# Kernel tuning notes

Measured on AMD Instinct MI355X. Metric: run time of the kernel, lower is better.

Reference implementation:

```python
import jax, jax.numpy as jnp
import numpy as np

NEG_SLOPE = 0.2  # PyG GATConv LeakyReLU slope
N_NODES = 50000
N_EDGES = 800000
F_IN, HID, HEADS, N_CLS = 166, 64, 8, 2


def setup_inputs() -> dict:
    key = jax.random.key(0)
    ks = jax.random.split(key, 16)
    s = 0.1
    return {
        "x": jax.random.normal(ks[0], (N_NODES, F_IN), jnp.float32),
        "edge_index": jax.random.randint(ks[1], (2, N_EDGES), 0, N_NODES, jnp.int64),
        "W1": jax.random.normal(ks[2], (F_IN, HEADS * HID), jnp.float32) * s,
        "a_src1": jax.random.normal(ks[3], (HEADS, HID), jnp.float32) * s,
        "a_dst1": jax.random.normal(ks[4], (HEADS, HID), jnp.float32) * s,
        "b1": jnp.zeros((HEADS * HID,), jnp.float32),
        # conv_final: 512 -> 64, 1 head, mean (concat=False)
        "W2": jax.random.normal(ks[5], (HEADS * HID, HID), jnp.float32) * s,
        "a_src2": jax.random.normal(ks[6], (1, HID), jnp.float32) * s,
        "a_dst2": jax.random.normal(ks[7], (1, HID), jnp.float32) * s,
        "b2": jnp.zeros((HID,), jnp.float32),
        # classifier MLP 64 -> 64 -> 2
        "Wc1": jax.random.normal(ks[8], (HID, HID), jnp.float32) * s,
        "bc1": jnp.zeros((HID,), jnp.float32),
        "Wc2": jax.random.normal(ks[9], (HID, N_CLS), jnp.float32) * s,
        "bc2": jnp.zeros((N_CLS,), jnp.float32),
    }


def gat_layer(x, src, dst, W, a_src, a_dst, b, concat):
    """PyG-style GATConv (eval mode, self-loops already in src/dst)."""
    N = x.shape[0]
    H, C = a_src.shape
    xp = (x @ W).reshape(N, H, C)                 # [N,H,C] projected features
    al_src = jnp.sum(xp * a_src, axis=-1)         # [N,H]
    al_dst = jnp.sum(xp * a_dst, axis=-1)         # [N,H]
    e = jax.nn.leaky_relu(al_src[src] + al_dst[dst], NEG_SLOPE)  # [E,H]
    # segment softmax over incoming edges of each target node
    m = jax.ops.segment_max(e, dst, num_segments=N)
    ex = jnp.exp(e - m[dst])
    denom = jax.ops.segment_sum(ex, dst, num_segments=N)
    alpha = ex / denom[dst]                       # [E,H]
    out = jax.ops.segment_sum(alpha[:, :, None] * xp[src], dst, num_segments=N)  # [N,H,C]
    out = out.reshape(N, H * C) if concat else out.mean(axis=1)
    return out + b


def reference(x, edge_index, W1, a_src1, a_dst1, b1, W2, a_src2, a_dst2, b2, Wc1, bc1, Wc2, bc2):
    N = x.shape[0]
    loops = jnp.arange(N, dtype=edge_index.dtype)
    src = jnp.concatenate([edge_index[0], loops])  # add self-loops (PyG default)
    dst = jnp.concatenate([edge_index[1], loops])
    h = jax.nn.elu(gat_layer(x, src, dst, W1, a_src1, a_dst1, b1, concat=True))
    h = gat_layer(h, src, dst, W2, a_src2, a_dst2, b2, concat=False)
    h = jax.nn.relu(h @ Wc1 + bc1)
    return h @ Wc2 + bc2
```

## Files before the change

kernel.cpp:

```cpp
#include <hip/hip_runtime.h>

#define NN   50000
#define E0   800000
#define ET   850000
#define FIN  166
#define KP1  192
#define HID  64
#define NH   8
#define F1   512
#define SCHUNK 52
#define DEGPAD (1024*SCHUNK)
#define G1BX 391
#define G1BLK (G1BX*4)
#define SCB  832

typedef __attribute__((ext_vector_type(8))) short short8;
typedef __attribute__((ext_vector_type(4))) float f32x4;
typedef __attribute__((ext_vector_type(4))) int int4v;
typedef unsigned short ush;

__device__ __forceinline__ float bf2f(unsigned short u){
  unsigned int x = ((unsigned int)u) << 16;
  return __builtin_bit_cast(float, x);
}
__device__ __forceinline__ unsigned short f2bf(float f){
  unsigned int x = __builtin_bit_cast(unsigned int, f);
  x += 0x7FFFu + ((x >> 16) & 1u);
  return (unsigned short)(x >> 16);
}

#define G1 (KP1/8)
#define T0V (NN*G1)
#define T1V (T0V + 512*G1)
#define T2V (T1V + 64*64)
#define T2W (T2V + 512)
#define T3V (T2W + ET)
__global__ __launch_bounds__(256) void k_prep_v(const float* __restrict__ x,
                                                const float* __restrict__ W1,
                                                const float* __restrict__ W2,
                                                const float* __restrict__ Wc1,
                                                const int* __restrict__ ei,
                                                ush* __restrict__ xpad,
                                                ush* __restrict__ W1t,
                                                ush* __restrict__ W2t,
                                                ush* __restrict__ Wc1t,
                                                int* __restrict__ deg){
  int i = blockIdx.x*256 + threadIdx.x;
  if (i >= T3V) return;
  if (i < T0V){
    int n = i / G1, g = i - n*G1, k0 = g*8;
    short8 o;
    #pragma unroll
    for (int j = 0; j < 8; j++){
      int k = k0 + j;
      o[j] = (short)f2bf(k < FIN ? x[(size_t)n*FIN + k] : 0.f);
    }
    *(short8*)(xpad + (size_t)n*KP1 + k0) = o;
  } else if (i < T1V){
    int j = i - T0V;
    int col = j / G1, g = j - col*G1, k0 = g*8;
    short8 o;
    #pragma unroll
    for (int q = 0; q < 8; q++){
      int k = k0 + q;
      o[q] = (short)f2bf(k < FIN ? W1[(size_t)k*512 + col] : 0.f);
    }
    *(short8*)(W1t + (size_t)col*KP1 + k0) = o;
  } else if (i < T2V){
    int j = i - T1V;
    int col = j >> 6, g = j & 63, k0 = g*8;
    short8 o;
    #pragma unroll
    for (int q = 0; q < 8; q++)
      o[q] = (short)f2bf(W2[(size_t)(k0 + q)*HID + col]);
    *(short8*)(W2t + (size_t)col*F1 + k0) = o;
  } else if (i < T2W){
    int j = i - T2V;
    int col = j >> 3, k0 = (j & 7)*8;
    short8 o;
    #pragma unroll
    for (int q = 0; q < 8; q++)
      o[q] = (short)f2bf(Wc1[(size_t)(k0 + q)*HID + col]);
    *(short8*)(Wc1t + (size_t)col*HID + k0) = o;
  } else {
    int e = i - T2W;
    int dst = (e < E0) ? ei[E0 + e] : (e - E0);
    atomicAdd(&deg[dst], 1);
  }
}

__global__ __launch_bounds__(1024) void k_scan(const int* __restrict__ deg,
                                               int* __restrict__ offs,
                                               int* __restrict__ cur){
  __shared__ int sums[1024];
  int t = threadIdx.x;
  for (int i = t; i < NN; i += 1024) cur[i] = 0;
  int base = t * SCHUNK;
  int4v v[13];
  int loc = 0;
  #pragma unroll
  for (int c = 0; c < 13; c++){
    v[c] = *(const int4v*)(deg + base + c*4);
    loc += v[c].x + v[c].y + v[c].z + v[c].w;
  }
  sums[t] = loc; __syncthreads();
  for (int off = 1; off < 1024; off <<= 1){
    int s = (t >= off) ? sums[t - off] : 0;
    __syncthreads();
    sums[t] += s;
    __syncthreads();
  }
  int run = sums[t] - loc;
  #pragma unroll
  for (int c = 0; c < 13; c++){
    int i0 = base + c*4;
    if (i0 + 0 < NN) offs[i0 + 0] = run;  run += v[c].x;
    if (i0 + 1 < NN) offs[i0 + 1] = run;  run += v[c].y;
    if (i0 + 2 < NN) offs[i0 + 2] = run;  run += v[c].z;
    if (i0 + 3 < NN) offs[i0 + 3] = run;  run += v[c].w;
  }
  if (t == 1023) offs[NN] = sums[1023];
}

__global__ __launch_bounds__(256) void k_sg1(const int* __restrict__ ei,
                                             const int* __restrict__ offs,
                                             int* __restrict__ cur,
                                             int* __restrict__ esrc,
                                             const ush* __restrict__ xpad,
                                             const ush* __restrict__ W1t,
                                             const float* __restrict__ a_s,
                                             const float* __restrict__ a_d,
                                             ush* __restrict__ xp1,
                                             float* __restrict__ als,
                                             float* __restrict__ ald){
  __shared__ ush As[128][40];
  __shared__ ush Bs[128][40];
  const int bid = blockIdx.x;
  if (bid >= G1BLK){
    int vb = bid - G1BLK;
    for (int e = vb*256 + (int)threadIdx.x; e < ET; e += SCB*256){
      int src, dst;
      if (e < E0){ src = ei[e]; dst = ei[E0 + e]; }
      else       { src = e - E0; dst = src; }
      int pos = offs[dst] + atomicAdd(&cur[dst], 1);
      esrc[pos] = src;
    }
    return;
  }
  const int m0 = (bid % G1BX)*128, n0 = (bid / G1BX)*128;
  const int t = threadIdx.x, wid = t>>6, l = t&63;
  const int wr = wid>>1, wc = wid&1;
  const int lr = l&15, ksl = (l>>4)*8;
  const int srow = t>>1, sc = (t&1)*16;

  f32x4 acc[4][4];
  #pragma unroll
  for (int m = 0; m < 4; m++)
    #pragma unroll
    for (int n = 0; n < 4; n++)
      #pragma unroll
      for (int j = 0; j < 4; j++) acc[m][n][j] = 0.f;

  const int gr = m0 + srow;
  const ush* Ap = xpad + (size_t)gr*KP1 + sc;
  const ush* Bp = W1t + (size_t)(n0 + srow)*KP1 + sc;

  for (int s = 0; s < 6; s++){
    const int kk = s*32;
    short8 a0, a1;
    #pragma unroll
    for (int j = 0; j < 8; j++){ a0[j] = 0; a1[j] = 0; }
    if (gr < NN){ a0 = *(const short8*)(Ap + kk); a1 = *(const short8*)(Ap + kk + 8); }
    short8 b0 = *(const short8*)(Bp + kk);
    short8 b1 = *(const short8*)(Bp + kk + 8);
    *(short8*)&As[srow][sc]   = a0;
    *(short8*)&As[srow][sc+8] = a1;
    *(short8*)&Bs[srow][sc]   = b0;
    *(short8*)&Bs[srow][sc+8] = b1;
    __syncthreads();
    short8 af[4], bfr[4];
    #pragma unroll
    for (int m = 0; m < 4; m++) af[m]  = *(const short8*)&As[wr*64 + m*16 + lr][ksl];
    #pragma unroll
    for (int n = 0; n < 4; n++) bfr[n] = *(const short8*)&Bs[wc*64 + n*16 + lr][ksl];
    #pragma unroll
    for (int m = 0; m < 4; m++)
      #pragma unroll
      for (int n = 0; n < 4; n++)
        acc[m][n] = __builtin_amdgcn_mfma_f32_16x16x32_bf16(af[m], bfr[n], acc[m][n], 0, 0, 0);
    __syncthreads();
  }

  #pragma unroll
  for (int m = 0; m < 4; m++)
    #pragma unroll
    for (int n = 0; n < 4; n++)
      #pragma unroll
      for (int j = 0; j < 4; j++){
        int row = m0 + wr*64 + m*16 + (l>>4)*4 + j;
        int col = n0 + wc*64 + n*16 + lr;
        if (row < NN) xp1[(size_t)row*F1 + col] = f2bf(acc[m][n][j]);
      }

  const int head = (bid / G1BX)*2 + wc;
  float asv[4], adv[4];
  #pragma unroll
  for (int n = 0; n < 4; n++){
    asv[n] = a_s[head*64 + n*16 + lr];
    adv[n] = a_d[head*64 + n*16 + lr];
  }
  #pragma unroll
  for (int m = 0; m < 4; m++)
    #pragma unroll
    for (int j = 0; j < 4; j++){
      float ps = 0.f, pd = 0.f;
      #pragma unroll
      for (int n = 0; n < 4; n++){
        ps = fmaf(acc[m][n][j], asv[n], ps);
        pd = fmaf(acc[m][n][j], adv[n], pd);
      }
      #pragma unroll
      for (int o = 1; o < 16; o <<= 1){
        ps += __shfl_xor(ps, o, 64);
        pd += __shfl_xor(pd, o, 64);
      }
      if (lr == 0){
        int row = m0 + wr*64 + m*16 + (l>>4)*4 + j;
        if (row < NN){
          als[(size_t)row*NH + head] = fminf(fmaxf(ps, -30.f), 30.f);
          ald[(size_t)row*NH + head] = fminf(fmaxf(pd, -30.f), 30.f);
        }
      }
    }
}

__global__ __launch_bounds__(256) void k_gemm2(const ush* __restrict__ h1,
                                               const ush* __restrict__ W2t,
                                               const float* __restrict__ a_s,
                                               const float* __restrict__ a_d,
                                               ush* __restrict__ xp2,
                                               float* __restrict__ als,
                                               float* __restrict__ ald){
  __shared__ ush As[128][40];
  __shared__ ush Bs[64][40];
  const int m0 = blockIdx.x*128;
  const int t = threadIdx.x, wid = t>>6, l = t&63;
  const int lr = l&15, ksl = (l>>4)*8;
  const int srow = t>>1, sc = (t&1)*16;

  f32x4 acc[2][4];
  #pragma unroll
  for (int m = 0; m < 2; m++)
    #pragma unroll
    for (int n = 0; n < 4; n++)
      #pragma unroll
      for (int j = 0; j < 4; j++) acc[m][n][j] = 0.f;

  const int gr = m0 + srow;
  const ush* Ap = h1 + (size_t)gr*F1 + sc;
  const ush* Bp = W2t + (size_t)srow*F1 + sc;

  for (int s = 0; s < 16; s++){
    const int kk = s*32;
    short8 a0, a1;
    #pragma unroll
    for (int j = 0; j < 8; j++){ a0[j] = 0; a1[j] = 0; }
    if (gr < NN){ a0 = *(const short8*)(Ap + kk); a1 = *(const short8*)(Ap + kk + 8); }
    *(short8*)&As[srow][sc]   = a0;
    *(short8*)&As[srow][sc+8] = a1;
    if (t < 128){
      short8 b0 = *(const short8*)(Bp + kk);
      short8 b1 = *(const short8*)(Bp + kk + 8);
      *(short8*)&Bs[srow][sc]   = b0;
      *(short8*)&Bs[srow][sc+8] = b1;
    }
    __syncthreads();
    short8 af[2], bfr[4];
    #pragma unroll
    for (int m = 0; m < 2; m++) af[m]  = *(const short8*)&As[wid*32 + m*16 + lr][ksl];
    #pragma unroll
    for (int n = 0; n < 4; n++) bfr[n] = *(const short8*)&Bs[n*16 + lr][ksl];
    #pragma unroll
    for (int m = 0; m < 2; m++)
      #pragma unroll
      for (int n = 0; n < 4; n++)
        acc[m][n] = __builtin_amdgcn_mfma_f32_16x16x32_bf16(af[m], bfr[n], acc[m][n], 0, 0, 0);
    __syncthreads();
  }

  #pragma unroll
  for (int m = 0; m < 2; m++)
    #pragma unroll
    for (int n = 0; n < 4; n++)
      #pragma unroll
      for (int j = 0; j < 4; j++){
        int row = m0 + wid*32 + m*16 + (l>>4)*4 + j;
        int col = n*16 + lr;
        if (row < NN) xp2[(size_t)row*HID + col] = f2bf(acc[m][n][j]);
      }

  float asv[4], adv[4];
  #pragma unroll
  for (int n = 0; n < 4; n++){
    asv[n] = a_s[n*16 + lr];
    adv[n] = a_d[n*16 + lr];
  }
  #pragma unroll
  for (int m = 0; m < 2; m++)
    #pragma unroll
    for (int j = 0; j < 4; j++){
      float ps = 0.f, pd = 0.f;
      #pragma unroll
      for (int n = 0; n < 4; n++){
        ps = fmaf(acc[m][n][j], asv[n], ps);
        pd = fmaf(acc[m][n][j], adv[n], pd);
      }
      #pragma unroll
      for (int o = 1; o < 16; o <<= 1){
        ps += __shfl_xor(ps, o, 64);
        pd += __shfl_xor(pd, o, 64);
      }
      if (lr == 0){
        int row = m0 + wid*32 + m*16 + (l>>4)*4 + j;
        if (row < NN){
          als[row] = fminf(fmaxf(ps, -30.f), 30.f);
          ald[row] = fminf(fmaxf(pd, -30.f), 30.f);
        }
      }
    }
}

__global__ __launch_bounds__(256) void k_agg1(const int* __restrict__ offs,
                                              const int* __restrict__ esrc,
                                              const ush* __restrict__ xp1,
                                              const float* __restrict__ als,
                                              const float* __restrict__ ald,
                                              const float* __restrict__ b1,
                                              ush* __restrict__ h1){
  int w = (blockIdx.x*256 + threadIdx.x) >> 6;
  int l = threadIdx.x & 63;
  if (w >= NN) return;
  int h = l >> 3;
  int f0 = l * 8;
  float ad = ald[w*NH + h];
  int s0 = offs[w], s1 = offs[w+1];
  float accA[8], accB[8];
  #pragma unroll
  for (int j = 0; j < 8; j++){ accA[j] = 0.f; accB[j] = 0.f; }
  float den = 0.f;

  for (int base = s0; base < s1; base += 64){
    int cnt = min(64, s1 - base);
    int myE = (base + l < s1) ? esrc[base + l] : 0;
    int j = 0;
    for (; j + 4 <= cnt; j += 4){
      int sA = __shfl(myE, j,   64);
      int sB = __shfl(myE, j+1, 64);
      int sC = __shfl(myE, j+2, 64);
      int sD = __shfl(myE, j+3, 64);
      float eA = als[sA*NH + h] + ad;
      float eB = als[sB*NH + h] + ad;
      float eC = als[sC*NH + h] + ad;
      float eD = als[sD*NH + h] + ad;
      eA = fmaxf(eA, 0.2f*eA); eB = fmaxf(eB, 0.2f*eB);
      eC = fmaxf(eC, 0.2f*eC); eD = fmaxf(eD, 0.2f*eD);
      float wA = __expf(eA), wB = __expf(eB), wC = __expf(eC), wD = __expf(eD);
      short8 vA = *(const short8*)(xp1 + (size_t)sA*F1 + f0);
      short8 vB = *(const short8*)(xp1 + (size_t)sB*F1 + f0);
      short8 vC = *(const short8*)(xp1 + (size_t)sC*F1 + f0);
      short8 vD = *(const short8*)(xp1 + (size_t)sD*F1 + f0);
      den += (wA + wB) + (wC + wD);
      #pragma unroll
      for (int jj = 0; jj < 8; jj++){
        accA[jj] = fmaf(wA, bf2f((ush)vA[jj]), accA[jj]);
        accB[jj] = fmaf(wB, bf2f((ush)vB[jj]), accB[jj]);
        accA[jj] = fmaf(wC, bf2f((ush)vC[jj]), accA[jj]);
        accB[jj] = fmaf(wD, bf2f((ush)vD[jj]), accB[jj]);
      }
    }
    for (; j < cnt; j++){
      int sA = __shfl(myE, j, 64);
      float eA = als[sA*NH + h] + ad;
      eA = fmaxf(eA, 0.2f*eA);
      float wA = __expf(eA);
      short8 vA = *(const short8*)(xp1 + (size_t)sA*F1 + f0);
      den += wA;
      #pragma unroll
      for (int jj = 0; jj < 8; jj++)
        accA[jj] = fmaf(wA, bf2f((ush)vA[jj]), accA[jj]);
    }
  }
  float inv = 1.f / den;
  #pragma unroll
  for (int jj = 0; jj < 8; jj++){
    float o = (accA[jj] + accB[jj])*inv + b1[f0 + jj];
    o = o > 0.f ? o : expm1f(o);
    h1[(size_t)w*F1 + f0 + jj] = f2bf(o);
  }
}

__global__ __launch_bounds__(256) void k_agg2(const int* __restrict__ offs,
                                              const int* __restrict__ esrc,
                                              const ush* __restrict__ xp2,
                                              const float* __restrict__ als,
                                              const float* __restrict__ ald,
                                              const float* __restrict__ b2,
                                              ush* __restrict__ h2g){
  int w = (blockIdx.x*256 + threadIdx.x) >> 6;
  int l = threadIdx.x & 63;
  if (w >= NN) return;
  float ad = ald[w];
  int s0 = offs[w], s1 = offs[w+1];
  float accA = 0.f, accB = 0.f, den = 0.f;

  for (int base = s0; base < s1; base += 64){
    int cnt = min(64, s1 - base);
    bool ok = (base + l < s1);
    int myE = ok ? esrc[base + l] : 0;
    float myW = 0.f;
    if (ok){
      float e_ = als[myE] + ad;
      e_ = fmaxf(e_, 0.2f*e_);
      myW = __expf(e_);
    }
    int j = 0;
    for (; j + 8 <= cnt; j += 8){
      int sA = __shfl(myE, j,   64), sB = __shfl(myE, j+1, 64);
      int sC = __shfl(myE, j+2, 64), sD = __shfl(myE, j+3, 64);
      int sE = __shfl(myE, j+4, 64), sF = __shfl(myE, j+5, 64);
      int sG = __shfl(myE, j+6, 64), sH = __shfl(myE, j+7, 64);
      float wA = __shfl(myW, j,   64), wB = __shfl(myW, j+1, 64);
      float wC = __shfl(myW, j+2, 64), wD = __shfl(myW, j+3, 64);
      float wE = __shfl(myW, j+4, 64), wF = __shfl(myW, j+5, 64);
      float wG = __shfl(myW, j+6, 64), wH = __shfl(myW, j+7, 64);
      float xA = bf2f(xp2[(size_t)sA*HID + l]);
      float xB = bf2f(xp2[(size_t)sB*HID + l]);
      float xC = bf2f(xp2[(size_t)sC*HID + l]);
      float xD = bf2f(xp2[(size_t)sD*HID + l]);
      float xE = bf2f(xp2[(size_t)sE*HID + l]);
      float xF = bf2f(xp2[(size_t)sF*HID + l]);
      float xG = bf2f(xp2[(size_t)sG*HID + l]);
      float xH = bf2f(xp2[(size_t)sH*HID + l]);
      den += ((wA + wB) + (wC + wD)) + ((wE + wF) + (wG + wH));
      accA = fmaf(wA, xA, accA); accB = fmaf(wB, xB, accB);
      accA = fmaf(wC, xC, accA); accB = fmaf(wD, xD, accB);
      accA = fmaf(wE, xE, accA); accB = fmaf(wF, xF, accB);
      accA = fmaf(wG, xG, accA); accB = fmaf(wH, xH, accB);
    }
    for (; j < cnt; j++){
      int sA = __shfl(myE, j, 64);
      float wA = __shfl(myW, j, 64);
      den += wA;
      accA = fmaf(wA, bf2f(xp2[(size_t)sA*HID + l]), accA);
    }
  }
  float h2 = (accA + accB) / den + b2[l];
  h2g[(size_t)w*HID + l] = f2bf(h2);
}

__global__ __launch_bounds__(256) void k_cls(const ush* __restrict__ h2g,
                                             const ush* __restrict__ Wc1t,
                                             const float* __restrict__ bc1,
                                             const float* __restrict__ Wc2,
                                             const float* __restrict__ bc2,
                                             float* __restrict__ out){
  const int t = threadIdx.x, wid = t>>6, l = t&63;
  const int lr = l&15, ksl = (l>>4)*8;
  const int m0 = blockIdx.x*128 + wid*32;

  f32x4 acc[2][4];
  #pragma unroll
  for (int m = 0; m < 2; m++)
    #pragma unroll
    for (int n = 0; n < 4; n++)
      #pragma unroll
      for (int j = 0; j < 4; j++) acc[m][n][j] = 0.f;

  #pragma unroll
  for (int ks = 0; ks < 2; ks++){
    short8 af[2], bfr[4];
    #pragma unroll
    for (int m = 0; m < 2; m++){
      int row = m0 + m*16 + lr;
      row = row < NN ? row : NN-1;
      af[m] = *(const short8*)(h2g + (size_t)row*HID + ks*32 + ksl);
    }
    #pragma unroll
    for (int n = 0; n < 4; n++)
      bfr[n] = *(const short8*)(Wc1t + (size_t)(n*16 + lr)*HID + ks*32 + ksl);
    #pragma unroll
    for (int m = 0; m < 2; m++)
      #pragma unroll
      for (int n = 0; n < 4; n++)
        acc[m][n] = __builtin_amdgcn_mfma_f32_16x16x32_bf16(af[m], bfr[n], acc[m][n], 0, 0, 0);
  }

  #pragma unroll
  for (int m = 0; m < 2; m++)
    #pragma unroll
    for (int j = 0; j < 4; j++){
      float q0 = 0.f, q1 = 0.f;
      #pragma unroll
      for (int n = 0; n < 4; n++){
        int col = n*16 + lr;
        float r = acc[m][n][j] + bc1[col];
        r = fmaxf(r, 0.f);
        q0 = fmaf(r, Wc2[col*2 + 0], q0);
        q1 = fmaf(r, Wc2[col*2 + 1], q1);
      }
      #pragma unroll
      for (int o = 1; o < 16; o <<= 1){
        q0 += __shfl_xor(q0, o, 64);
        q1 += __shfl_xor(q1, o, 64);
      }
      if (lr == 0){
        int row = m0 + m*16 + (l>>4)*4 + j;
        if (row < NN){
          out[(size_t)row*2 + 0] = q0 + bc2[0];
          out[(size_t)row*2 + 1] = q1 + bc2[1];
        }
      }
    }
}

extern "C" void kernel_launch(void* const* d_in, const int* in_sizes, int n_in,
                              void* d_out, int out_size, void* d_ws, size_t ws_size,
                              hipStream_t stream){
  const float* x   = (const float*)d_in[0];
  const int*   ei  = (const int*)  d_in[1];
  const float* W1  = (const float*)d_in[2];
  const float* as1 = (const float*)d_in[3];
  const float* ad1 = (const float*)d_in[4];
  const float* b1  = (const float*)d_in[5];
  const float* W2  = (const float*)d_in[6];
  const float* as2 = (const float*)d_in[7];
  const float* ad2 = (const float*)d_in[8];
  const float* b2  = (const float*)d_in[9];
  const float* Wc1 = (const float*)d_in[10];
  const float* bc1 = (const float*)d_in[11];
  const float* Wc2 = (const float*)d_in[12];
  const float* bc2 = (const float*)d_in[13];
  float* out = (float*)d_out;

  char* p = (char*)d_ws; size_t off = 0;
  auto alloc = [&](size_t b){ void* r = p + off; off = (off + b + 255) & ~(size_t)255; return r; };
  ush* xpad = (ush*)alloc((size_t)NN*KP1*2);
  ush* W1t  = (ush*)alloc((size_t)512*KP1*2);
  ush* W2t  = (ush*)alloc((size_t)HID*F1*2);
  ush* Wc1t = (ush*)alloc((size_t)HID*HID*2);
  ush* xp1  = (ush*)alloc((size_t)NN*F1*2);
  ush* h1   = (ush*)alloc((size_t)NN*F1*2);
  ush* xp2  = (ush*)alloc((size_t)NN*HID*2);
  ush* h2g  = (ush*)alloc((size_t)NN*HID*2);
  float* als1 = (float*)alloc((size_t)NN*NH*4);
  float* ald1 = (float*)alloc((size_t)NN*NH*4);
  float* als2 = (float*)alloc((size_t)NN*4);
  float* ald2 = (float*)alloc((size_t)NN*4);
  int* deg  = (int*)alloc((size_t)DEGPAD*4);
  int* cur  = (int*)alloc((size_t)NN*4);
  int* offs = (int*)alloc((size_t)(NN+1)*4);
  int* esrc = (int*)alloc((size_t)ET*4);

  hipMemsetAsync(deg, 0, (size_t)DEGPAD*4, stream);

  k_prep_v<<<(T3V + 255)/256, 256, 0, stream>>>(x, W1, W2, Wc1, ei, xpad, W1t, W2t, Wc1t, deg);
  k_scan<<<1, 1024, 0, stream>>>(deg, offs, cur);
  k_sg1<<<G1BLK + SCB, 256, 0, stream>>>(ei, offs, cur, esrc,
                                         xpad, W1t, as1, ad1, xp1, als1, ald1);
  k_agg1<<<12500, 256, 0, stream>>>(offs, esrc, xp1, als1, ald1, b1, h1);

  k_gemm2<<<391, 256, 0, stream>>>(h1, W2t, as2, ad2, xp2, als2, ald2);
  k_agg2<<<12500, 256, 0, stream>>>(offs, esrc, xp2, als2, ald2, b2, h2g);
  k_cls<<<391, 256, 0, stream>>>(h2g, Wc1t, bc1, Wc2, bc2, out);
}
```

Before: 371.6 us.

## Preload full weight tile to LDS and stream A fragments directly from global

Both GEMM kernels now load the entire weight slice (all K) into shared memory once, then read A-operand MFMA fragments straight from global memory into registers. This removes the per-k-step LDS staging of A and the two barriers per iteration. Out-of-range rows are clamped to the last row instead of zero-filled, which is safe because those rows are never stored. The trade-off is more shared memory per block (about 50KB for gemm1 and 66KB for gemm2), which may lower occupancy, and uncoalesced-ish global loads for A with no reuse across waves.

```diff
diff --git a/kernel.cpp b/kernel.cpp
--- a/kernel.cpp
+++ b/kernel.cpp
@@ -133,8 +133,7 @@
                                              ush* __restrict__ xp1,
                                              float* __restrict__ als,
                                              float* __restrict__ ald){
-  __shared__ ush As[128][40];
-  __shared__ ush Bs[128][40];
+  __shared__ ush Bs[128][200];
   const int bid = blockIdx.x;
   if (bid >= G1BLK){
     int vb = bid - G1BLK;
@@ -153,6 +152,18 @@
   const int lr = l&15, ksl = (l>>4)*8;
   const int srow = t>>1, sc = (t&1)*16;
 
+  {
+    const ush* Bp = W1t + (size_t)(n0 + srow)*KP1;
+    #pragma unroll
+    for (int c = 0; c < 6; c++){
+      short8 b0 = *(const short8*)(Bp + c*32 + sc);
+      short8 b1 = *(const short8*)(Bp + c*32 + sc + 8);
+      *(short8*)&Bs[srow][c*32 + sc]     = b0;
+      *(short8*)&Bs[srow][c*32 + sc + 8] = b1;
+    }
+  }
+  __syncthreads();
+
   f32x4 acc[4][4];
   #pragma unroll
   for (int m = 0; m < 4; m++)
@@ -161,34 +172,27 @@
       #pragma unroll
       for (int j = 0; j < 4; j++) acc[m][n][j] = 0.f;
 
-  const int gr = m0 + srow;
-  const ush* Ap = xpad + (size_t)gr*KP1 + sc;
-  const ush* Bp = W1t + (size_t)(n0 + srow)*KP1 + sc;
+  int arow[4];
+  #pragma unroll
+  for (int m = 0; m < 4; m++){
+    int r = m0 + wr*64 + m*16 + lr;
+    arow[m] = r < NN ? r : NN-1;
+  }
 
   for (int s = 0; s < 6; s++){
     const int kk = s*32;
-    short8 a0, a1;
-    #pragma unroll
-    for (int j = 0; j < 8; j++){ a0[j] = 0; a1[j] = 0; }
-    if (gr < NN){ a0 = *(const short8*)(Ap + kk); a1 = *(const short8*)(Ap + kk + 8); }
-    short8 b0 = *(const short8*)(Bp + kk);
-    short8 b1 = *(const short8*)(Bp + kk + 8);
-    *(short8*)&As[srow][sc]   = a0;
-    *(short8*)&As[srow][sc+8] = a1;
-    *(short8*)&Bs[srow][sc]   = b0;
-    *(short8*)&Bs[srow][sc+8] = b1;
-    __syncthreads();
     short8 af[4], bfr[4];
     #pragma unroll
-    for (int m = 0; m < 4; m++) af[m]  = *(const short8*)&As[wr*64 + m*16 + lr][ksl];
-    #pragma unroll
-    for (int n = 0; n < 4; n++) bfr[n] = *(const short8*)&Bs[wc*64 + n*16 + lr][ksl];
+    for (int m = 0; m < 4; m++)
+      af[m] = *(const short8*)(xpad + (size_t)arow[m]*KP1 + kk + ksl);
+    #pragma unroll
+    for (int n = 0; n < 4; n++)
+      bfr[n] = *(const short8*)&Bs[wc*64 + n*16 + lr][kk + ksl];
     #pragma unroll
     for (int m = 0; m < 4; m++)
       #pragma unroll
       for (int n = 0; n < 4; n++)
         acc[m][n] = __builtin_amdgcn_mfma_f32_16x16x32_bf16(af[m], bfr[n], acc[m][n], 0, 0, 0);
-    __syncthreads();
   }
 
   #pragma unroll
@@ -241,12 +245,21 @@
                                                ush* __restrict__ xp2,
                                                float* __restrict__ als,
                                                float* __restrict__ ald){
-  __shared__ ush As[128][40];
-  __shared__ ush Bs[64][40];
+  __shared__ ush Bs[64][520];
   const int m0 = blockIdx.x*128;
   const int t = threadIdx.x, wid = t>>6, l = t&63;
   const int lr = l&15, ksl = (l>>4)*8;
-  const int srow = t>>1, sc = (t&1)*16;
+
+  {
+    const int br = t>>2, bq = (t&3)*128;
+    const ush* Bp = W2t + (size_t)br*F1 + bq;
+    #pragma unroll
+    for (int c = 0; c < 16; c++){
+      short8 b = *(const short8*)(Bp + c*8);
+      *(short8*)&Bs[br][bq + c*8] = b;
+    }
+  }
+  __syncthreads();
 
   f32x4 acc[2][4];
   #pragma unroll
@@ -256,36 +269,27 @@
       #pragma unroll
       for (int j = 0; j < 4; j++) acc[m][n][j] = 0.f;
 
-  const int gr = m0 + srow;
-  const ush* Ap = h1 + (size_t)gr*F1 + sc;
-  const ush* Bp = W2t + (size_t)srow*F1 + sc;
+  int arow[2];
+  #pragma unroll
+  for (int m = 0; m < 2; m++){
+    int r = m0 + wid*32 + m*16 + lr;
+    arow[m] = r < NN ? r : NN-1;
+  }
 
   for (int s = 0; s < 16; s++){
     const int kk = s*32;
-    short8 a0, a1;
-    #pragma unroll
-    for (int j = 0; j < 8; j++){ a0[j] = 0; a1[j] = 0; }
-    if (gr < NN){ a0 = *(const short8*)(Ap + kk); a1 = *(const short8*)(Ap + kk + 8); }
-    *(short8*)&As[srow][sc]   = a0;
-    *(short8*)&As[srow][sc+8] = a1;
-    if (t < 128){
-      short8 b0 = *(const short8*)(Bp + kk);
-      short8 b1 = *(const short8*)(Bp + kk + 8);
-      *(short8*)&Bs[srow][sc]   = b0;
-      *(short8*)&Bs[srow][sc+8] = b1;
-    }
-    __syncthreads();
     short8 af[2], bfr[4];
     #pragma unroll
-    for (int m = 0; m < 2; m++) af[m]  = *(const short8*)&As[wid*32 + m*16 + lr][ksl];
-    #pragma unroll
-    for (int n = 0; n < 4; n++) bfr[n] = *(const short8*)&Bs[n*16 + lr][ksl];
+    for (int m = 0; m < 2; m++)
+      af[m] = *(const short8*)(h1 + (size_t)arow[m]*F1 + kk + ksl);
+    #pragma unroll
+    for (int n = 0; n < 4; n++)
+      bfr[n] = *(const short8*)&Bs[n*16 + lr][kk + ksl];
     #pragma unroll
     for (int m = 0; m < 2; m++)
       #pragma unroll
       for (int n = 0; n < 4; n++)
         acc[m][n] = __builtin_amdgcn_mfma_f32_16x16x32_bf16(af[m], bfr[n], acc[m][n], 0, 0, 0);
-    __syncthreads();
   }
 
   #pragma unroll
```

After: 371.4 us. Within noise of the previous version (-0.0%).
